# Kernel optimization log

Measured on AMD Instinct MI355X. Metric: run time of the kernel, lower is better.

The kernel has to match this reference:

```python
import jax, jax.numpy as jnp
import numpy as np

B, L, S, DIM, NH = 4, 1024, 1024, 1024, 16
DH = DIM // NH


def setup_inputs() -> dict:
    key = jax.random.key(0)
    ks = jax.random.split(key, 16)
    std = 0.02
    inp = {
        'q': jax.random.normal(ks[0], (B, L, DIM), jnp.float32),
        'k': jax.random.normal(ks[1], (B, S, DIM), jnp.float32),
        'v': jax.random.normal(ks[2], (B, S, DIM), jnp.float32),
        'attn_mask': jax.random.bernoulli(ks[3], 0.9, (B, L, S)),
        'pos_bias': jax.random.normal(ks[4], (B, NH, L, S), jnp.float32),
        'Wq': jax.random.normal(ks[5], (DIM, DIM), jnp.float32) * std,
        'bq': jnp.zeros((DIM,), jnp.float32),
        'Wk': jax.random.normal(ks[6], (DIM, DIM), jnp.float32) * std,
        'bk': jnp.zeros((DIM,), jnp.float32),
        'Wv': jax.random.normal(ks[7], (DIM, DIM), jnp.float32) * std,
        'bv': jnp.zeros((DIM,), jnp.float32),
        'Wp': jax.random.normal(ks[8], (DIM, DIM), jnp.float32) * std,
        'bp': jnp.zeros((DIM,), jnp.float32),
        'is_causal': 1,
    }
    return inp


def _attention(q, k, v, attn_mask, pos_bias, Wq, bq, Wk, bk, Wv, bv, Wp, bp, is_causal):
    b, l, _ = q.shape
    s = k.shape[1]
    qh = (q @ Wq + bq).reshape(b, l, NH, DH)   # (B,L,nH,dh)
    kh = (k @ Wk + bk).reshape(b, s, NH, DH)
    vh = (v @ Wv + bv).reshape(b, s, NH, DH)

    mask = attn_mask  # (B,L,S) bool
    if is_causal:
        causal = jnp.tril(jnp.ones((l, l), dtype=bool))
        causal = jnp.pad(causal, ((0, 0), (s - l, 0)), constant_values=True)  # (L,S)
        mask = mask & causal[None]
    # rows with no allowed key attend everywhere (matches torch row-fix)
    row_any = mask.any(axis=-1, keepdims=True)
    mask = jnp.where(row_any, mask, True)

    bias = jnp.where(mask[:, None, :, :], pos_bias, -jnp.inf)  # (B,nH,L,S)
    scale = 1.0 / np.sqrt(DH).astype(np.float32)
    scores = jnp.einsum('blhd,bshd->bhls', qh, kh) * scale + bias
    attn = jax.nn.softmax(scores, axis=-1)
    o = jnp.einsum('bhls,bshd->blhd', attn, vh).reshape(b, l, NH * DH)
    return o @ Wp + bp


def reference(q, k, v, attn_mask, pos_bias, Wq, bq, Wk, bk, Wv, bv, Wp, bp, is_causal):
    return _attention(q, k, v, attn_mask, pos_bias, Wq, bq, Wk, bk, Wv, bv, Wp, bp, is_causal)
```

## Files before the change

kernel.cpp:

```cpp
#include <hip/hip_runtime.h>
#include <hip/hip_bf16.h>

typedef __hip_bfloat16 bf16;
typedef __attribute__((ext_vector_type(4))) float  floatx4;
typedef __attribute__((ext_vector_type(8))) short  short8;
typedef __attribute__((ext_vector_type(8))) __bf16 bf16x8;

constexpr int Bc = 4, Lc = 1024, Sc = 1024, DIMc = 1024, NHc = 16, DHc = 64;

template <typename V>
__device__ auto mfma_bf16_sel(V a, V b, floatx4 c, int)
    -> decltype(__builtin_amdgcn_mfma_f32_16x16x32_bf16(a, b, c, 0, 0, 0)) {
  return __builtin_amdgcn_mfma_f32_16x16x32_bf16(a, b, c, 0, 0, 0);
}
template <typename V>
__device__ floatx4 mfma_bf16_sel(V a, V b, floatx4 c, long) {
  bf16x8 a2 = __builtin_bit_cast(bf16x8, a);
  bf16x8 b2 = __builtin_bit_cast(bf16x8, b);
  return __builtin_amdgcn_mfma_f32_16x16x32_bf16(a2, b2, c, 0, 0, 0);
}
__device__ inline floatx4 mfma_bf16(short8 a, short8 b, floatx4 c) {
  return mfma_bf16_sel(a, b, c, 0);
}

union U8 { uint4 u; bf16 h[8]; };

__device__ inline U8 load8(const float* p) {
    float4 f0 = ((const float4*)p)[0];
    float4 f1 = ((const float4*)p)[1];
    U8 t;
    t.h[0] = __float2bfloat16(f0.x); t.h[1] = __float2bfloat16(f0.y);
    t.h[2] = __float2bfloat16(f0.z); t.h[3] = __float2bfloat16(f0.w);
    t.h[4] = __float2bfloat16(f1.x); t.h[5] = __float2bfloat16(f1.y);
    t.h[6] = __float2bfloat16(f1.z); t.h[7] = __float2bfloat16(f1.w);
    return t;
}
__device__ inline void store_elem(float* p, float v) { *p = v; }
__device__ inline void store_elem(bf16*  p, float v) { *p = __float2bfloat16(v); }

__global__ __launch_bounds__(256)
void prep_kernel(const float* __restrict__ q, const float* __restrict__ k,
                 const float* __restrict__ v,
                 const float* __restrict__ Wq, const float* __restrict__ Wk,
                 const float* __restrict__ Wv, const float* __restrict__ Wp,
                 bf16* __restrict__ qb, bf16* __restrict__ kb,
                 bf16* __restrict__ vb,
                 bf16* __restrict__ wqt, bf16* __restrict__ wkt,
                 bf16* __restrict__ wvt, bf16* __restrict__ wpt)
{
    __shared__ float tile[64][68];
    const int tid = threadIdx.x;
    int blk = blockIdx.x;

    if (blk < 6144) {
        const float* src = (blk < 2048) ? q : (blk < 4096) ? k : v;
        bf16*        dst = (blk < 2048) ? qb : (blk < 4096) ? kb : vb;
        const int off = (blk & 2047) * 2048 + tid * 8;
        U8 t = load8(src + off);
        *(uint4*)(dst + off) = t.u;
    } else {
        blk -= 6144;
        const int w  = blk >> 8, t2 = blk & 255;
        const float* W  = (w == 0) ? Wq : (w == 1) ? Wk : (w == 2) ? Wv : Wp;
        bf16*        Wt = (w == 0) ? wqt : (w == 1) ? wkt : (w == 2) ? wvt : wpt;
        const int tk = (t2 >> 4) << 6;
        const int tn = (t2 & 15) << 6;
        #pragma unroll
        for (int i = 0; i < 4; ++i) {
            const int r = (tid >> 4) + i * 16;
            const int c = (tid & 15) << 2;
            *(float4*)(&tile[r][c]) =
                *(const float4*)(W + (size_t)(tk + r) * DIMc + tn + c);
        }
        __syncthreads();
        #pragma unroll
        for (int j = 0; j < 2; ++j) {
            const int nn = tid >> 2;
            const int kc = (tid & 3) + j * 4;
            U8 o;
            #pragma unroll
            for (int u = 0; u < 8; ++u)
                o.h[u] = __float2bfloat16(tile[kc * 8 + u][nn]);
            *(uint4*)(Wt + (size_t)(tn + nn) * DIMc + tk + kc * 8) = o.u;
        }
    }
}

constexpr int GPAD = 72;

template <typename TO>
__global__ __launch_bounds__(256)
void gemm_bt_kernel(const bf16* __restrict__ A, const bf16* __restrict__ Bt,
                    const float* __restrict__ bias, TO* __restrict__ out,
                    int mode)
{
    __shared__ bf16 As[128 * GPAD];
    __shared__ bf16 Bs[128 * GPAD];

    const int tid  = threadIdx.x;
    const int wave = tid >> 6;
    const int lane = tid & 63;
    const int n = lane & 15, g = lane >> 4;
    const int m0 = blockIdx.x * 128;
    const int n0 = blockIdx.y * 128;
    const int wq_m = (wave & 1) * 64, wq_n = (wave >> 1) * 64;

    floatx4 acc[4][4];
    #pragma unroll
    for (int a = 0; a < 4; ++a)
        #pragma unroll
        for (int b2 = 0; b2 < 4; ++b2)
            acc[a][b2] = (floatx4){0.f, 0.f, 0.f, 0.f};

    const int srow   = tid >> 3;
    const int schunk = (tid & 7) * 8;

    for (int k0 = 0; k0 < DIMc; k0 += 64) {
        #pragma unroll
        for (int i = 0; i < 4; ++i) {
            const int r = srow + i * 32;
            *(uint4*)(&As[r * GPAD + schunk]) =
                *(const uint4*)(A + (size_t)(m0 + r) * DIMc + k0 + schunk);
            *(uint4*)(&Bs[r * GPAD + schunk]) =
                *(const uint4*)(Bt + (size_t)(n0 + r) * DIMc + k0 + schunk);
        }
        __syncthreads();
        #pragma unroll
        for (int ks = 0; ks < 2; ++ks) {
            short8 af[4], bf_[4];
            #pragma unroll
            for (int t = 0; t < 4; ++t) {
                af[t]  = *(const short8*)(&As[(wq_m + t * 16 + n) * GPAD + ks * 32 + g * 8]);
                bf_[t] = *(const short8*)(&Bs[(wq_n + t * 16 + n) * GPAD + ks * 32 + g * 8]);
            }
            #pragma unroll
            for (int tm = 0; tm < 4; ++tm)
                #pragma unroll
                for (int tn = 0; tn < 4; ++tn)
                    acc[tm][tn] = mfma_bf16(af[tm], bf_[tn], acc[tm][tn]);
        }
        __syncthreads();
    }

    #pragma unroll
    for (int tn = 0; tn < 4; ++tn) {
        const int col = n0 + wq_n + tn * 16 + n;
        const float bval = bias[col];
        #pragma unroll
        for (int tm = 0; tm < 4; ++tm) {
            #pragma unroll
            for (int r = 0; r < 4; ++r) {
                const int row = m0 + wq_m + tm * 16 + g * 4 + r;
                const float vv = acc[tm][tn][r] + bval;
                const int bb = row >> 10, ll = row & (Lc - 1);
                const int hh = col >> 6,  dd = col & 63;
                size_t idx;
                if (mode == 0)      idx = (size_t)row * DIMc + col;
                else if (mode == 1) idx = (((size_t)(bb * NHc + hh) * Lc + ll) * DHc) + dd;
                else                idx = (((size_t)(bb * NHc + hh) * DHc + dd) * Sc) + ll;
                store_elem(out + idx, vv);
            }
        }
    }
}

constexpr int PADk = 72;

__global__ __launch_bounds__(256)
void flash_attn_kernel(const bf16* __restrict__ qh, const bf16* __restrict__ kh,
                       const bf16* __restrict__ vt, const int* __restrict__ mask,
                       const float* __restrict__ pos_bias,
                       const int* __restrict__ is_causal_p, bf16* __restrict__ o)
{
    __shared__ bf16 Ks[64 * PADk];
    __shared__ bf16 Vs[64 * PADk];
    __shared__ bf16 Pw[4][16 * PADk];
    __shared__ int rowany[64];
    __shared__ int hasfix_s;

    const int tid  = threadIdx.x;
    const int lane = tid & 63;
    const int wave = tid >> 6;
    const int n = lane & 15;
    const int g = lane >> 4;

    const int qt = blockIdx.x & 15;
    const int bh = blockIdx.x >> 4;
    const int h  = bh & (NHc - 1);
    const int b  = bh >> 4;
    const int l0 = qt * 64;
    const bool causal = (is_causal_p[0] != 0);

    if (tid < 64) rowany[tid] = 0;
    if (tid == 0) hasfix_s = 0;
    __syncthreads();
    {
        const int row = tid >> 2, part = tid & 3;
        const int l = l0 + row;
        const int limit = causal ? l : (Sc - 1);
        const int* mrow = mask + ((size_t)b * Lc + l) * Sc;
        int any = 0;
        for (int s = part * 256; s < part * 256 + 256; ++s) {
            if (s <= limit && mrow[s] != 0) { any = 1; break; }
        }
        if (any) atomicOr(&rowany[row], 1);
    }
    __syncthreads();
    if (tid < 64 && rowany[tid] == 0) atomicOr(&hasfix_s, 1);
    __syncthreads();
    const bool hasfix = (hasfix_s != 0);

    const int qrow_frag = l0 + wave * 16 + n;
    const bf16* qp = qh + ((size_t)bh * Lc + qrow_frag) * DHc;
    const short8 qf0 = *(const short8*)(qp + g * 8);
    const short8 qf1 = *(const short8*)(qp + 32 + g * 8);

    floatx4 oacc[4];
    #pragma unroll
    for (int t = 0; t < 4; ++t) oacc[t] = (floatx4){0.f, 0.f, 0.f, 0.f};
    float m_run[4], l_run[4];
    #pragma unroll
    for (int r = 0; r < 4; ++r) { m_run[r] = -3.0e38f; l_run[r] = 0.f; }

    int nchunk = Sc / 64;
    if (causal && !hasfix) nchunk = qt + 1;

    for (int c = 0; c < nchunk; ++c) {
        const int s0 = c * 64;
        __syncthreads();
        #pragma unroll
        for (int it = 0; it < 2; ++it) {
            const int e  = tid * 8 + it * 2048;
            const int r0 = e >> 6, c0 = e & 63;
            *(uint4*)(Ks + r0 * PADk + c0) =
                *(const uint4*)(kh + ((size_t)bh * Sc + s0 + r0) * DHc + c0);
            *(uint4*)(Vs + r0 * PADk + c0) =
                *(const uint4*)(vt + ((size_t)bh * DHc + r0) * Sc + s0 + c0);
        }
        __syncthreads();

        float bi[4][4]; int mk[4][4];
        #pragma unroll
        for (int r = 0; r < 4; ++r) {
            const int l = l0 + wave * 16 + g * 4 + r;
            const size_t mb = ((size_t)b  * Lc + l) * Sc + s0 + n;
            const size_t pb = ((size_t)bh * Lc + l) * Sc + s0 + n;
            #pragma unroll
            for (int t = 0; t < 4; ++t) {
                mk[r][t] = mask[mb + 16 * t];
                bi[r][t] = pos_bias[pb + 16 * t];
            }
        }

        floatx4 scv[4];
        #pragma unroll
        for (int t = 0; t < 4; ++t) scv[t] = (floatx4){0.f, 0.f, 0.f, 0.f};
        #pragma unroll
        for (int t = 0; t < 4; ++t) {
            short8 kb0 = *(const short8*)(Ks + (16 * t + n) * PADk + g * 8);
            short8 kb1 = *(const short8*)(Ks + (16 * t + n) * PADk + 32 + g * 8);
            scv[t] = mfma_bf16(qf0, kb0, scv[t]);
            scv[t] = mfma_bf16(qf1, kb1, scv[t]);
        }

        #pragma unroll
        for (int r = 0; r < 4; ++r) {
            const int row = wave * 16 + g * 4 + r;
            const int l = l0 + row;
            const int limit = causal ? l : (Sc - 1);
            const bool fix = (rowany[row] == 0);
            float vals[4];
            #pragma unroll
            for (int t = 0; t < 4; ++t) {
                const int s = s0 + 16 * t + n;
                const bool ok = fix || (s <= limit && mk[r][t] != 0);
                vals[t] = ok ? scv[t][r] * 0.125f + bi[r][t] : -3.0e38f;
            }
            float cm = fmaxf(fmaxf(vals[0], vals[1]), fmaxf(vals[2], vals[3]));
            cm = fmaxf(cm, __shfl_xor(cm, 1));
            cm = fmaxf(cm, __shfl_xor(cm, 2));
            cm = fmaxf(cm, __shfl_xor(cm, 4));
            cm = fmaxf(cm, __shfl_xor(cm, 8));
            const float mnew = fmaxf(m_run[r], cm);
            const float alpha = __expf(m_run[r] - mnew);
            float csum = 0.f;
            #pragma unroll
            for (int t = 0; t < 4; ++t) {
                const float p = (vals[t] < -1.0e37f) ? 0.f : __expf(vals[t] - mnew);
                csum += p;
                Pw[wave][row % 16 * PADk + 16 * t + n] = __float2bfloat16(p);
            }
            csum += __shfl_xor(csum, 1);
            csum += __shfl_xor(csum, 2);
            csum += __shfl_xor(csum, 4);
            csum += __shfl_xor(csum, 8);
            l_run[r] = l_run[r] * alpha + csum;
            m_run[r] = mnew;
            #pragma unroll
            for (int t = 0; t < 4; ++t) oacc[t][r] *= alpha;
        }
        __syncthreads();

        #pragma unroll
        for (int sc2 = 0; sc2 < 2; ++sc2) {
            short8 pa = *(const short8*)(Pw[wave] + n * PADk + sc2 * 32 + g * 8);
            #pragma unroll
            for (int t = 0; t < 4; ++t) {
                short8 vb = *(const short8*)(Vs + (16 * t + n) * PADk + sc2 * 32 + g * 8);
                oacc[t] = mfma_bf16(pa, vb, oacc[t]);
            }
        }
    }

    #pragma unroll
    for (int r = 0; r < 4; ++r) {
        const int l = l0 + wave * 16 + g * 4 + r;
        const float inv = 1.f / l_run[r];
        #pragma unroll
        for (int t = 0; t < 4; ++t) {
            const int d = 16 * t + n;
            o[((size_t)(b * Lc + l)) * DIMc + h * DHc + d] =
                __float2bfloat16(oacc[t][r] * inv);
        }
    }
}

extern "C" void kernel_launch(void* const* d_in, const int* in_sizes, int n_in,
                              void* d_out, int out_size, void* d_ws, size_t ws_size,
                              hipStream_t stream)
{
    (void)in_sizes; (void)n_in; (void)out_size; (void)ws_size;

    const float* q        = (const float*)d_in[0];
    const float* k        = (const float*)d_in[1];
    const float* v        = (const float*)d_in[2];
    const int*   mask     = (const int*)d_in[3];
    const float* pos_bias = (const float*)d_in[4];
    const float* Wq = (const float*)d_in[5];
    const float* bq = (const float*)d_in[6];
    const float* Wk = (const float*)d_in[7];
    const float* bk = (const float*)d_in[8];
    const float* Wv = (const float*)d_in[9];
    const float* bv = (const float*)d_in[10];
    const float* Wp = (const float*)d_in[11];
    const float* bp = (const float*)d_in[12];
    const int*   is_causal = (const int*)d_in[13];

    const size_t per = (size_t)Bc * NHc * Lc * DHc;
    const size_t wsz = (size_t)DIMc * DIMc;
    bf16* qh  = (bf16*)d_ws;
    bf16* kh  = qh + per;
    bf16* vt  = kh + per;
    bf16* oh  = vt + per;
    bf16* qb  = oh + per;
    bf16* kb  = qb + per;
    bf16* vb  = kb + per;
    bf16* wqt = vb + per;
    bf16* wkt = wqt + wsz;
    bf16* wvt = wkt + wsz;
    bf16* wpt = wvt + wsz;
    float* outp = (float*)d_out;

    dim3 bb(256);

    prep_kernel<<<7168, bb, 0, stream>>>(q, k, v, Wq, Wk, Wv, Wp,
                                         qb, kb, vb, wqt, wkt, wvt, wpt);

    dim3 gg(32, 8);
    gemm_bt_kernel<bf16><<<gg, bb, 0, stream>>>(qb, wqt, bq, qh, 1);
    gemm_bt_kernel<bf16><<<gg, bb, 0, stream>>>(kb, wkt, bk, kh, 1);
    gemm_bt_kernel<bf16><<<gg, bb, 0, stream>>>(vb, wvt, bv, vt, 2);

    flash_attn_kernel<<<(Bc * NHc) * (Lc / 64), bb, 0, stream>>>(
        qh, kh, vt, mask, pos_bias, is_causal, oh);

    gemm_bt_kernel<float><<<gg, bb, 0, stream>>>(oh, wpt, bp, outp, 0);
}
```

Measured before the change: 599.9 us.

## Fuse input bf16 cast into QKV GEMM, bit-pack mask, vectorize bias loads

The separate fp32-to-bf16 conversion pass over q/k/v is removed. The QKV GEMM now loads fp32 directly and converts on the fly, and the three projections are merged into one launch via grid z. The prep kernel packs the int mask into 64-bit bitmasks and precomputes per-row any-allowed flags, so the attention kernel no longer rescans the full int mask per tile or reads 4-byte mask entries. Score columns are permuted so each lane reads pos_bias as float4 and writes P as packed uint2, and one __syncthreads in the inner loop is dropped. The risks are extra fp32 global traffic in the GEMM loads and correctness depending on the per-wave Pw buffer not needing the removed barrier.

```diff
diff --git a/kernel.cpp b/kernel.cpp
--- a/kernel.cpp
+++ b/kernel.cpp
@@ -35,31 +35,21 @@
     t.h[6] = __float2bfloat16(f1.z); t.h[7] = __float2bfloat16(f1.w);
     return t;
 }
-__device__ inline void store_elem(float* p, float v) { *p = v; }
-__device__ inline void store_elem(bf16*  p, float v) { *p = __float2bfloat16(v); }
 
 __global__ __launch_bounds__(256)
-void prep_kernel(const float* __restrict__ q, const float* __restrict__ k,
-                 const float* __restrict__ v,
-                 const float* __restrict__ Wq, const float* __restrict__ Wk,
+void prep_kernel(const float* __restrict__ Wq, const float* __restrict__ Wk,
                  const float* __restrict__ Wv, const float* __restrict__ Wp,
-                 bf16* __restrict__ qb, bf16* __restrict__ kb,
-                 bf16* __restrict__ vb,
+                 const int* __restrict__ mask, const int* __restrict__ is_causal_p,
                  bf16* __restrict__ wqt, bf16* __restrict__ wkt,
-                 bf16* __restrict__ wvt, bf16* __restrict__ wpt)
+                 bf16* __restrict__ wvt, bf16* __restrict__ wpt,
+                 unsigned long long* __restrict__ mbits,
+                 int* __restrict__ rowany_g)
 {
     __shared__ float tile[64][68];
     const int tid = threadIdx.x;
     int blk = blockIdx.x;
 
-    if (blk < 6144) {
-        const float* src = (blk < 2048) ? q : (blk < 4096) ? k : v;
-        bf16*        dst = (blk < 2048) ? qb : (blk < 4096) ? kb : vb;
-        const int off = (blk & 2047) * 2048 + tid * 8;
-        U8 t = load8(src + off);
-        *(uint4*)(dst + off) = t.u;
-    } else {
-        blk -= 6144;
+    if (blk < 1024) {
         const int w  = blk >> 8, t2 = blk & 255;
         const float* W  = (w == 0) ? Wq : (w == 1) ? Wk : (w == 2) ? Wv : Wp;
         bf16*        Wt = (w == 0) ? wqt : (w == 1) ? wkt : (w == 2) ? wvt : wpt;
@@ -83,19 +73,59 @@
                 o.h[u] = __float2bfloat16(tile[kc * 8 + u][nn]);
             *(uint4*)(Wt + (size_t)(tn + nn) * DIMc + tk + kc * 8) = o.u;
         }
+    } else {
+        const int mb  = blk - 1024;
+        const int rIb = tid >> 4;
+        const int w   = tid & 15;
+        const int row = mb * 16 + rIb;
+        const int l   = row & (Lc - 1);
+        const bool causal = (is_causal_p[0] != 0);
+
+        const int4* mr4 = (const int4*)(mask + (size_t)row * Sc + w * 64);
+        unsigned long long bits = 0ull;
+        #pragma unroll
+        for (int i = 0; i < 16; ++i) {
+            int4 m4 = mr4[i];
+            unsigned long long nib =
+                (unsigned long long)((m4.x != 0) | ((m4.y != 0) << 1) |
+                                     ((m4.z != 0) << 2) | ((m4.w != 0) << 3));
+            bits |= nib << (4 * i);
+        }
+        mbits[(size_t)row * 16 + w] = bits;
+
+        const int limit = causal ? l : (Sc - 1);
+        const int base  = w * 64;
+        unsigned long long am;
+        if (limit >= base + 63)  am = bits;
+        else if (limit < base)   am = 0ull;
+        else                     am = bits & ((2ull << (limit - base)) - 1ull);
+        unsigned long long red = am;
+        #pragma unroll
+        for (int d2 = 1; d2 < 16; d2 <<= 1) red |= __shfl_xor(red, d2);
+        if (w == 0) rowany_g[row] = (red != 0ull) ? 1 : 0;
     }
 }
 
 constexpr int GPAD = 72;
 
-template <typename TO>
 __global__ __launch_bounds__(256)
-void gemm_bt_kernel(const bf16* __restrict__ A, const bf16* __restrict__ Bt,
-                    const float* __restrict__ bias, TO* __restrict__ out,
-                    int mode)
+void gemm_qkv_kernel(const float* __restrict__ q, const float* __restrict__ k,
+                     const float* __restrict__ v,
+                     const bf16* __restrict__ wqt, const bf16* __restrict__ wkt,
+                     const bf16* __restrict__ wvt,
+                     const float* __restrict__ bq, const float* __restrict__ bk,
+                     const float* __restrict__ bv,
+                     bf16* __restrict__ qh, bf16* __restrict__ kh,
+                     bf16* __restrict__ vt)
 {
     __shared__ bf16 As[128 * GPAD];
     __shared__ bf16 Bs[128 * GPAD];
+
+    const int z = blockIdx.z;
+    const float* A    = (z == 0) ? q   : (z == 1) ? k   : v;
+    const bf16*  Bt   = (z == 0) ? wqt : (z == 1) ? wkt : wvt;
+    const float* bias = (z == 0) ? bq  : (z == 1) ? bk  : bv;
+    bf16*        out  = (z == 0) ? qh  : (z == 1) ? kh  : vt;
 
     const int tid  = threadIdx.x;
     const int wave = tid >> 6;
@@ -119,8 +149,8 @@
         #pragma unroll
         for (int i = 0; i < 4; ++i) {
             const int r = srow + i * 32;
-            *(uint4*)(&As[r * GPAD + schunk]) =
-                *(const uint4*)(A + (size_t)(m0 + r) * DIMc + k0 + schunk);
+            U8 a8 = load8(A + (size_t)(m0 + r) * DIMc + k0 + schunk);
+            *(uint4*)(&As[r * GPAD + schunk]) = a8.u;
             *(uint4*)(&Bs[r * GPAD + schunk]) =
                 *(const uint4*)(Bt + (size_t)(n0 + r) * DIMc + k0 + schunk);
         }
@@ -155,10 +185,76 @@
                 const int bb = row >> 10, ll = row & (Lc - 1);
                 const int hh = col >> 6,  dd = col & 63;
                 size_t idx;
-                if (mode == 0)      idx = (size_t)row * DIMc + col;
-                else if (mode == 1) idx = (((size_t)(bb * NHc + hh) * Lc + ll) * DHc) + dd;
-                else                idx = (((size_t)(bb * NHc + hh) * DHc + dd) * Sc) + ll;
-                store_elem(out + idx, vv);
+                if (z < 2) idx = (((size_t)(bb * NHc + hh) * Lc + ll) * DHc) + dd;
+                else       idx = (((size_t)(bb * NHc + hh) * DHc + dd) * Sc) + ll;
+                out[idx] = __float2bfloat16(vv);
+            }
+        }
+    }
+}
+
+__global__ __launch_bounds__(256)
+void gemm_out_kernel(const bf16* __restrict__ A, const bf16* __restrict__ Bt,
+                     const float* __restrict__ bias, float* __restrict__ out)
+{
+    __shared__ bf16 As[128 * GPAD];
+    __shared__ bf16 Bs[128 * GPAD];
+
+    const int tid  = threadIdx.x;
+    const int wave = tid >> 6;
+    const int lane = tid & 63;
+    const int n = lane & 15, g = lane >> 4;
+    const int m0 = blockIdx.x * 128;
+    const int n0 = blockIdx.y * 128;
+    const int wq_m = (wave & 1) * 64, wq_n = (wave >> 1) * 64;
+
+    floatx4 acc[4][4];
+    #pragma unroll
+    for (int a = 0; a < 4; ++a)
+        #pragma unroll
+        for (int b2 = 0; b2 < 4; ++b2)
+            acc[a][b2] = (floatx4){0.f, 0.f, 0.f, 0.f};
+
+    const int srow   = tid >> 3;
+    const int schunk = (tid & 7) * 8;
+
+    for (int k0 = 0; k0 < DIMc; k0 += 64) {
+        #pragma unroll
+        for (int i = 0; i < 4; ++i) {
+            const int r = srow + i * 32;
+            *(uint4*)(&As[r * GPAD + schunk]) =
+                *(const uint4*)(A + (size_t)(m0 + r) * DIMc + k0 + schunk);
+            *(uint4*)(&Bs[r * GPAD + schunk]) =
+                *(const uint4*)(Bt + (size_t)(n0 + r) * DIMc + k0 + schunk);
+        }
+        __syncthreads();
+        #pragma unroll
+        for (int ks = 0; ks < 2; ++ks) {
+            short8 af[4], bf_[4];
+            #pragma unroll
+            for (int t = 0; t < 4; ++t) {
+                af[t]  = *(const short8*)(&As[(wq_m + t * 16 + n) * GPAD + ks * 32 + g * 8]);
+                bf_[t] = *(const short8*)(&Bs[(wq_n + t * 16 + n) * GPAD + ks * 32 + g * 8]);
+            }
+            #pragma unroll
+            for (int tm = 0; tm < 4; ++tm)
+                #pragma unroll
+                for (int tn = 0; tn < 4; ++tn)
+                    acc[tm][tn] = mfma_bf16(af[tm], bf_[tn], acc[tm][tn]);
+        }
+        __syncthreads();
+    }
+
+    #pragma unroll
+    for (int tn = 0; tn < 4; ++tn) {
+        const int col = n0 + wq_n + tn * 16 + n;
+        const float bval = bias[col];
+        #pragma unroll
+        for (int tm = 0; tm < 4; ++tm) {
+            #pragma unroll
+            for (int r = 0; r < 4; ++r) {
+                const int row = m0 + wq_m + tm * 16 + g * 4 + r;
+                out[(size_t)row * DIMc + col] = acc[tm][tn][r] + bval;
             }
         }
     }
@@ -168,7 +264,9 @@
 
 __global__ __launch_bounds__(256)
 void flash_attn_kernel(const bf16* __restrict__ qh, const bf16* __restrict__ kh,
-                       const bf16* __restrict__ vt, const int* __restrict__ mask,
+                       const bf16* __restrict__ vt,
+                       const unsigned long long* __restrict__ mbits,
+                       const int* __restrict__ rowany_g,
                        const float* __restrict__ pos_bias,
                        const int* __restrict__ is_causal_p, bf16* __restrict__ o)
 {
@@ -191,22 +289,13 @@
     const int l0 = qt * 64;
     const bool causal = (is_causal_p[0] != 0);
 
-    if (tid < 64) rowany[tid] = 0;
     if (tid == 0) hasfix_s = 0;
     __syncthreads();
-    {
-        const int row = tid >> 2, part = tid & 3;
-        const int l = l0 + row;
-        const int limit = causal ? l : (Sc - 1);
-        const int* mrow = mask + ((size_t)b * Lc + l) * Sc;
-        int any = 0;
-        for (int s = part * 256; s < part * 256 + 256; ++s) {
-            if (s <= limit && mrow[s] != 0) { any = 1; break; }
-        }
-        if (any) atomicOr(&rowany[row], 1);
-    }
-    __syncthreads();
-    if (tid < 64 && rowany[tid] == 0) atomicOr(&hasfix_s, 1);
+    if (tid < 64) {
+        const int ra = rowany_g[(b << 10) + l0 + tid];
+        rowany[tid] = ra;
+        if (ra == 0) atomicOr(&hasfix_s, 1);
+    }
     __syncthreads();
     const bool hasfix = (hasfix_s != 0);
 
@@ -239,17 +328,15 @@
         }
         __syncthreads();
 
-        float bi[4][4]; int mk[4][4];
+        float bvv[4][4]; int nib[4];
         #pragma unroll
         for (int r = 0; r < 4; ++r) {
             const int l = l0 + wave * 16 + g * 4 + r;
-            const size_t mb = ((size_t)b  * Lc + l) * Sc + s0 + n;
-            const size_t pb = ((size_t)bh * Lc + l) * Sc + s0 + n;
-            #pragma unroll
-            for (int t = 0; t < 4; ++t) {
-                mk[r][t] = mask[mb + 16 * t];
-                bi[r][t] = pos_bias[pb + 16 * t];
-            }
+            const float4 b4 =
+                *(const float4*)(pos_bias + ((size_t)bh * Lc + l) * Sc + s0 + 4 * n);
+            bvv[r][0] = b4.x; bvv[r][1] = b4.y; bvv[r][2] = b4.z; bvv[r][3] = b4.w;
+            const unsigned long long wbits = mbits[((size_t)(b << 10) + l) * 16 + c];
+            nib[r] = (int)((wbits >> (4 * n)) & 15ull);
         }
 
         floatx4 scv[4];
@@ -257,8 +344,9 @@
         for (int t = 0; t < 4; ++t) scv[t] = (floatx4){0.f, 0.f, 0.f, 0.f};
         #pragma unroll
         for (int t = 0; t < 4; ++t) {
-            short8 kb0 = *(const short8*)(Ks + (16 * t + n) * PADk + g * 8);
-            short8 kb1 = *(const short8*)(Ks + (16 * t + n) * PADk + 32 + g * 8);
+            const bf16* kp = Ks + (4 * n + t) * PADk + g * 8;
+            short8 kb0 = *(const short8*)(kp);
+            short8 kb1 = *(const short8*)(kp + 32);
             scv[t] = mfma_bf16(qf0, kb0, scv[t]);
             scv[t] = mfma_bf16(qf1, kb1, scv[t]);
         }
@@ -272,9 +360,9 @@
             float vals[4];
             #pragma unroll
             for (int t = 0; t < 4; ++t) {
-                const int s = s0 + 16 * t + n;
-                const bool ok = fix || (s <= limit && mk[r][t] != 0);
-                vals[t] = ok ? scv[t][r] * 0.125f + bi[r][t] : -3.0e38f;
+                const int s = s0 + 4 * n + t;
+                const bool ok = fix || (s <= limit && ((nib[r] >> t) & 1));
+                vals[t] = ok ? scv[t][r] * 0.125f + bvv[r][t] : -3.0e38f;
             }
             float cm = fmaxf(fmaxf(vals[0], vals[1]), fmaxf(vals[2], vals[3]));
             cm = fmaxf(cm, __shfl_xor(cm, 1));
@@ -284,12 +372,14 @@
             const float mnew = fmaxf(m_run[r], cm);
             const float alpha = __expf(m_run[r] - mnew);
             float csum = 0.f;
+            union PK { uint2 u; bf16 hb[4]; } pk;
             #pragma unroll
             for (int t = 0; t < 4; ++t) {
                 const float p = (vals[t] < -1.0e37f) ? 0.f : __expf(vals[t] - mnew);
                 csum += p;
-                Pw[wave][row % 16 * PADk + 16 * t + n] = __float2bfloat16(p);
-            }
+                pk.hb[t] = __float2bfloat16(p);
+            }
+            *(uint2*)(&Pw[wave][(row & 15) * PADk + 4 * n]) = pk.u;
             csum += __shfl_xor(csum, 1);
             csum += __shfl_xor(csum, 2);
             csum += __shfl_xor(csum, 4);
@@ -299,7 +389,6 @@
             #pragma unroll
             for (int t = 0; t < 4; ++t) oacc[t][r] *= alpha;
         }
-        __syncthreads();
 
         #pragma unroll
         for (int sc2 = 0; sc2 < 2; ++sc2) {
@@ -352,27 +441,26 @@
     bf16* kh  = qh + per;
     bf16* vt  = kh + per;
     bf16* oh  = vt + per;
-    bf16* qb  = oh + per;
-    bf16* kb  = qb + per;
-    bf16* vb  = kb + per;
-    bf16* wqt = vb + per;
+    bf16* wqt = oh + per;
     bf16* wkt = wqt + wsz;
     bf16* wvt = wkt + wsz;
     bf16* wpt = wvt + wsz;
+    unsigned long long* mbits = (unsigned long long*)(wpt + wsz);
+    int* rowany_g = (int*)(mbits + (size_t)Bc * Lc * 16);
     float* outp = (float*)d_out;
 
     dim3 bb(256);
 
-    prep_kernel<<<7168, bb, 0, stream>>>(q, k, v, Wq, Wk, Wv, Wp,
-                                         qb, kb, vb, wqt, wkt, wvt, wpt);
+    prep_kernel<<<1280, bb, 0, stream>>>(Wq, Wk, Wv, Wp, mask, is_causal,
+                                         wqt, wkt, wvt, wpt, mbits, rowany_g);
+
+    dim3 gq(32, 8, 3);
+    gemm_qkv_kernel<<<gq, bb, 0, stream>>>(q, k, v, wqt, wkt, wvt,
+                                           bq, bk, bv, qh, kh, vt);
+
+    flash_attn_kernel<<<(Bc * NHc) * (Lc / 64), bb, 0, stream>>>(
+        qh, kh, vt, mbits, rowany_g, pos_bias, is_causal, oh);
 
     dim3 gg(32, 8);
-    gemm_bt_kernel<bf16><<<gg, bb, 0, stream>>>(qb, wqt, bq, qh, 1);
-    gemm_bt_kernel<bf16><<<gg, bb, 0, stream>>>(kb, wkt, bk, kh, 1);
-    gemm_bt_kernel<bf16><<<gg, bb, 0, stream>>>(vb, wvt, bv, vt, 2);
-
-    flash_attn_kernel<<<(Bc * NHc) * (Lc / 64), bb, 0, stream>>>(
-        qh, kh, vt, mask, pos_bias, is_causal, oh);
-
-    gemm_bt_kernel<float><<<gg, bb, 0, stream>>>(oh, wpt, bp, outp, 0);
-}
+    gemm_out_kernel<<<gg, bb, 0, stream>>>(oh, wpt, bp, outp);
+}
```

Measured after the change: 589.5 us. About the same (-1.7%).
